# Kernel tuning notes

Hardware: AMD Instinct MI355X
Metric: run time of the kernel (lower is better)

## Reference

```python
import jax, jax.numpy as jnp
import numpy as np

# ---- pywt filter banks (dec_lo, dec_hi, rec_lo, rec_hi), all pywt-ordered ----
_SQ2 = 0.7071067811865476

def _orth(dec_lo):
    dec_lo = np.asarray(dec_lo, dtype=np.float64)
    rec_lo = dec_lo[::-1].copy()
    k = np.arange(len(dec_lo))
    dec_hi = ((-1.0) ** (k + 1)) * rec_lo
    rec_hi = dec_hi[::-1].copy()
    return dec_lo, dec_hi, rec_lo, rec_hi

_DB4 = [-0.010597401784997278, 0.032883011666982945, 0.030841381835986965,
        -0.18703481171888114, -0.02798376941698385, 0.6308807679295904,
        0.7148465705525415, 0.23037781330885523]
_SYM6 = [-0.007800708325034148, 0.0017677118642428036, 0.04472490177066578,
         -0.021060292512300564, -0.07263752278646252, 0.3379294217276218,
         0.787641141030194, 0.4910559419267466, -0.048311742585633,
         -0.11799011114819057, 0.0034907120842174702, 0.015404109327027373]
_BIOR13 = (
    np.array([-0.08838834764831845, 0.08838834764831845, _SQ2, _SQ2, 0.08838834764831845, -0.08838834764831845]),
    np.array([0.0, 0.0, -_SQ2, _SQ2, 0.0, 0.0]),
    np.array([0.0, 0.0, _SQ2, _SQ2, 0.0, 0.0]),
    np.array([-0.08838834764831845, -0.08838834764831845, _SQ2, -_SQ2, 0.08838834764831845, 0.08838834764831845]),
)

WAVELETS = ['haar', 'db4', 'sym6', 'bior1.3']
FILTERS = {
    'haar': _orth([_SQ2, _SQ2]),
    'db4': _orth(_DB4),
    'sym6': _orth(_SYM6),
    'bior1.3': _BIOR13,
}
FILTERS = {k: tuple(jnp.asarray(f, dtype=jnp.float32) for f in v) for k, v in FILTERS.items()}


def _dwt(x, dec_lo, dec_hi):
    # x: [B, C, T] (T even). ptwt: reflect-pad (2L-3)//2 each side, stride-2 corr with flipped dec filters.
    B, C, T = x.shape
    L = dec_lo.shape[0]
    p = (2 * L - 3) // 2
    xp = jnp.pad(x, ((0, 0), (0, 0), (p, p)), mode='reflect') if p > 0 else x
    filt = jnp.stack([dec_lo[::-1], dec_hi[::-1]])[:, None, :].astype(x.dtype)  # [2,1,L]
    out = jax.lax.conv_general_dilated(
        xp.reshape(B * C, 1, -1), filt, window_strides=(2,), padding='VALID',
        dimension_numbers=('NCH', 'OIH', 'NCH'))
    out = out.reshape(B, C, 2, -1)
    return out[:, :, 0], out[:, :, 1]  # approx, detail: [B, C, (T+L-2)//2]


def _idwt(lo, hi, rec_lo, rec_hi):
    # conv_transpose stride 2 with rec filters, then crop (2L-3)//2 per side (ptwt waverec).
    B, C, Tc = lo.shape
    L = rec_lo.shape[0]
    p = (2 * L - 3) // 2
    c = jnp.stack([lo, hi], axis=2).reshape(B * C, 2, Tc)
    filt = jnp.stack([rec_lo[::-1], rec_hi[::-1]])[None].astype(lo.dtype)  # [1,2,L]
    y = jax.lax.conv_general_dilated(
        c, filt, window_strides=(1,), padding=[(L - 1, L - 1)],
        lhs_dilation=(2,), dimension_numbers=('NCH', 'OIH', 'NCH'))
    y = y.reshape(B, C, -1)
    if p > 0:
        y = y[:, :, p:-p]
    return y


def _spectral(z, lam, gamma, cos_theta):
    return gamma * jnp.sign(z) * jax.nn.relu(jnp.abs(z) - lam) * cos_theta


def setup_inputs() -> dict:
    key = jax.random.key(0)
    ks = jax.random.split(key, 8)
    B, S, E = 8, 4096, 1024
    x = jax.random.normal(ks[0], (B, S, E), dtype=jnp.float32)
    lambda_approx = jnp.full((1, E, 1), 0.05, jnp.float32) + 0.01 * jax.random.uniform(ks[1], (1, E, 1), jnp.float32)
    lambda_detail = jnp.full((1, E, 1), 0.05, jnp.float32) + 0.01 * jax.random.uniform(ks[2], (1, E, 1), jnp.float32)
    log_gamma = 0.1 * jax.random.normal(ks[3], (1, E, 1), jnp.float32)
    theta = 0.1 * jax.random.normal(ks[4], (1, E, 1), jnp.float32)
    basis_logits = 0.5 * jax.random.normal(ks[5], (4,), jnp.float32)
    ln_weight = jnp.ones((E,), jnp.float32)
    ln_bias = jnp.zeros((E,), jnp.float32)
    return {'x': x, 'lambda_approx': lambda_approx, 'lambda_detail': lambda_detail,
            'log_gamma': log_gamma, 'theta': theta, 'basis_logits': basis_logits,
            'ln_weight': ln_weight, 'ln_bias': ln_bias}


def reference(x, lambda_approx, lambda_detail, log_gamma, theta, basis_logits, ln_weight, ln_bias):
    residual = x                       # [B, S, E]
    S = x.shape[1]
    xt = jnp.transpose(x, (0, 2, 1))   # [B, E, S]
    gamma = jax.nn.softplus(log_gamma) + 1e-6
    ct = jnp.cos(theta)
    weights = jax.nn.softmax(basis_logits)  # all 4 wavelets valid for even S
    out = jnp.zeros_like(xt)
    for i, name in enumerate(WAVELETS):
        dl, dh, rl, rh = FILTERS[name]
        lo, hi = _dwt(xt, dl, dh)
        lo = _spectral(lo, lambda_approx, gamma, ct)
        hi = _spectral(hi, lambda_detail, gamma, ct)
        rec = _idwt(lo, hi, rl, rh)[:, :, :S]
        out = out + weights[i] * rec
    y = jnp.transpose(out, (0, 2, 1)) + residual
    mu = jnp.mean(y, axis=-1, keepdims=True)
    var = jnp.var(y, axis=-1, keepdims=True)
    return (y - mu) / jnp.sqrt(var + 1e-5) * ln_weight + ln_bias
```

## Files before the change

### kernel.cpp

```cpp
#include <hip/hip_runtime.h>
#include <cstdint>

#define T_SEQ 4096
#define E_DIM 1024
#define N_B   8
#define SC    64
#define TILE_P 84
typedef float v2f __attribute__((ext_vector_type(2)));

constexpr int LW[4] = {2, 8, 12, 6};

constexpr float DLf[4][12] = {
  {0.7071067811865476f, 0.7071067811865476f, 0,0,0,0,0,0,0,0,0,0},
  {-0.010597401784997278f, 0.032883011666982945f, 0.030841381835986965f, -0.18703481171888114f,
   -0.02798376941698385f, 0.6308807679295904f, 0.7148465705525415f, 0.23037781330885523f, 0,0,0,0},
  {-0.007800708325034148f, 0.0017677118642428036f, 0.04472490177066578f, -0.021060292512300564f,
   -0.07263752278646252f, 0.3379294217276218f, 0.787641141030194f, 0.4910559419267466f,
   -0.048311742585633f, -0.11799011114819057f, 0.0034907120842174702f, 0.015404109327027373f},
  {-0.08838834764831845f, 0.08838834764831845f, 0.7071067811865476f, 0.7071067811865476f,
    0.08838834764831845f, -0.08838834764831845f, 0,0,0,0,0,0},
};
constexpr float DHf[4][12] = {
  {-0.7071067811865476f, 0.7071067811865476f, 0,0,0,0,0,0,0,0,0,0},
  {-0.23037781330885523f, 0.7148465705525415f, -0.6308807679295904f, -0.02798376941698385f,
    0.18703481171888114f, 0.030841381835986965f, -0.032883011666982945f, -0.010597401784997278f, 0,0,0,0},
  {-0.015404109327027373f, 0.0034907120842174702f, 0.11799011114819057f, -0.048311742585633f,
   -0.4910559419267466f, 0.787641141030194f, -0.3379294217276218f, -0.07263752278646252f,
    0.021060292512300564f, 0.04472490177066578f, -0.0017677118642428036f, -0.007800708325034148f},
  {0,0,-0.7071067811865476f, 0.7071067811865476f, 0,0, 0,0,0,0,0,0},
};
constexpr float RLf[4][12] = {
  {0.7071067811865476f, 0.7071067811865476f, 0,0,0,0,0,0,0,0,0,0},
  {0.23037781330885523f, 0.7148465705525415f, 0.6308807679295904f, -0.02798376941698385f,
   -0.18703481171888114f, 0.030841381835986965f, 0.032883011666982945f, -0.010597401784997278f, 0,0,0,0},
  {0.015404109327027373f, 0.0034907120842174702f, -0.11799011114819057f, -0.048311742585633f,
   0.4910559419267466f, 0.787641141030194f, 0.3379294217276218f, -0.07263752278646252f,
   -0.021060292512300564f, 0.04472490177066578f, 0.0017677118642428036f, -0.007800708325034148f},
  {0,0,0.7071067811865476f, 0.7071067811865476f, 0,0, 0,0,0,0,0,0},
};
constexpr float RHf[4][12] = {
  {0.7071067811865476f, -0.7071067811865476f, 0,0,0,0,0,0,0,0,0,0},
  {-0.010597401784997278f, -0.032883011666982945f, 0.030841381835986965f, 0.18703481171888114f,
   -0.02798376941698385f, -0.6308807679295904f, 0.7148465705525415f, -0.23037781330885523f, 0,0,0,0},
  {-0.007800708325034148f, -0.0017677118642428036f, 0.04472490177066578f, 0.021060292512300564f,
   -0.07263752278646252f, -0.3379294217276218f, 0.787641141030194f, -0.4910559419267466f,
   -0.048311742585633f, 0.11799011114819057f, 0.0034907120842174702f, -0.015404109327027373f},
  {-0.08838834764831845f, -0.08838834764831845f, 0.7071067811865476f, -0.7071067811865476f,
    0.08838834764831845f, 0.08838834764831845f, 0,0,0,0,0,0},
};

__device__ __forceinline__ v2f sv(float c) { return v2f{c, c}; }

template <int W>
__device__ __forceinline__ void wavelet_accum(const v2f (&xw)[36], v2f (&acc)[16],
                                              v2f la, v2f ld, v2f gw) {
  constexpr int L  = LW[W];
  constexpr int KT = L / 2 + 7;
#pragma unroll
  for (int kk = 0; kk < KT; ++kk) {
    v2f lo = {0.f, 0.f}, hi = {0.f, 0.f};
#pragma unroll
    for (int m = 0; m < L; ++m) {
      const v2f xv = xw[2 * kk + 11 - m];
      if (DLf[W][m] != 0.0f) lo += sv(DLf[W][m]) * xv;
      if (DHf[W][m] != 0.0f) hi += sv(DHf[W][m]) * xv;
    }
    v2f cl, ch;
    cl.x = __builtin_amdgcn_fmed3f(lo.x, -la.x, la.x);
    cl.y = __builtin_amdgcn_fmed3f(lo.y, -la.y, la.y);
    ch.x = __builtin_amdgcn_fmed3f(hi.x, -ld.x, ld.x);
    ch.y = __builtin_amdgcn_fmed3f(hi.y, -ld.y, ld.y);
    const v2f loS = (lo - cl) * gw;
    const v2f hiS = (hi - ch) * gw;
#pragma unroll
    for (int m = 0; m < L; ++m) {
      const int j = 2 * kk + m + 2 - L;
      if (j >= 0 && j < 16) {
        if (RLf[W][m] != 0.0f) acc[j] += loS * sv(RLf[W][m]);
        if (RHf[W][m] != 0.0f) acc[j] += hiS * sv(RHf[W][m]);
      }
    }
  }
}

__global__ __launch_bounds__(256, 3) void wlm_k1(
    const float* __restrict__ x,
    const float* __restrict__ la_, const float* __restrict__ ld_,
    const float* __restrict__ lg_, const float* __restrict__ th_,
    const float* __restrict__ bl_, float* __restrict__ y) {
  __shared__ float xs[TILE_P][2][64];

  const int tid  = threadIdx.x;
  const int lane = tid & 63;
  const int wave = tid >> 6;
  const int s0 = blockIdx.x * SC;
  const int e0 = blockIdx.y * 128;
  const int b  = blockIdx.z;

  {
    const int c4  = (tid & 31) * 4;
    const int sel = c4 >> 6;
    const int cc  = c4 & 63;
    const int prow = tid >> 5;
#pragma unroll
    for (int it = 0; it < 11; ++it) {
      const int pos = prow + it * 8;
      if (pos < TILE_P) {
        int g = s0 - 10 + pos;
        g = (g < 0) ? -g : g;
        g = (g >= T_SEQ) ? (2 * T_SEQ - 2 - g) : g;
        const float4 v = *reinterpret_cast<const float4*>(
            &x[((size_t)b * T_SEQ + g) * E_DIM + e0 + c4]);
        *reinterpret_cast<float4*>(&xs[pos][sel][cc]) = v;
      }
    }
  }

  const int e = e0 + lane, e2 = e + 64;
  const v2f la = {la_[e], la_[e2]};
  const v2f ld = {ld_[e], ld_[e2]};
  const v2f lg = {lg_[e], lg_[e2]};
  const v2f th = {th_[e], th_[e2]};
  v2f g2;
  g2.x = (fmaxf(lg.x, 0.f) + log1pf(expf(-fabsf(lg.x))) + 1e-6f) * cosf(th.x);
  g2.y = (fmaxf(lg.y, 0.f) + log1pf(expf(-fabsf(lg.y))) + 1e-6f) * cosf(th.y);

  const float b0 = bl_[0], b1 = bl_[1], b2 = bl_[2], b3 = bl_[3];
  const float mx = fmaxf(fmaxf(b0, b1), fmaxf(b2, b3));
  const float w0 = expf(b0 - mx), w1 = expf(b1 - mx),
              w2 = expf(b2 - mx), w3 = expf(b3 - mx);
  const float wr = 1.f / (w0 + w1 + w2 + w3);
  const v2f gw0 = g2 * sv(w0 * wr), gw1 = g2 * sv(w1 * wr),
            gw2 = g2 * sv(w2 * wr), gw3 = g2 * sv(w3 * wr);

  __syncthreads();

  const int base = wave * 16;
  v2f xw[36];
#pragma unroll
  for (int i = 0; i < 36; ++i) {
    xw[i] = v2f{xs[base + i][0][lane], xs[base + i][1][lane]};
  }

  v2f acc[16];
#pragma unroll
  for (int j = 0; j < 16; ++j) acc[j] = v2f{0.f, 0.f};

  wavelet_accum<0>(xw, acc, la, ld, gw0);
  wavelet_accum<1>(xw, acc, la, ld, gw1);
  wavelet_accum<2>(xw, acc, la, ld, gw2);
  wavelet_accum<3>(xw, acc, la, ld, gw3);

  const int sA = s0 + wave * 16;
#pragma unroll
  for (int j = 0; j < 16; ++j) {
    const v2f o = xw[j + 10] + acc[j];
    const size_t off = ((size_t)b * T_SEQ + sA + j) * E_DIM + e;
    y[off]      = o.x;
    y[off + 64] = o.y;
  }
}

__global__ __launch_bounds__(256) void wlm_k2(float* __restrict__ y,
                                              const float* __restrict__ w,
                                              const float* __restrict__ bias) {
  const int token = blockIdx.x;
  const int tid = threadIdx.x;
  float* row = y + (size_t)token * E_DIM;

  float4 v = *reinterpret_cast<const float4*>(&row[tid * 4]);
  float s  = v.x + v.y + v.z + v.w;
  float sq = v.x * v.x + v.y * v.y + v.z * v.z + v.w * v.w;
#pragma unroll
  for (int off = 32; off; off >>= 1) {
    s  += __shfl_down(s, off);
    sq += __shfl_down(sq, off);
  }
  __shared__ float ps[4], pq[4], stat[2];
  const int wave = tid >> 6, lane = tid & 63;
  if (lane == 0) { ps[wave] = s; pq[wave] = sq; }
  __syncthreads();
  if (tid == 0) {
    const float S1 = ps[0] + ps[1] + ps[2] + ps[3];
    const float S2 = pq[0] + pq[1] + pq[2] + pq[3];
    const float mu = S1 * (1.f / E_DIM);
    const float var = S2 * (1.f / E_DIM) - mu * mu;
    stat[0] = mu;
    stat[1] = rsqrtf(var + 1e-5f);
  }
  __syncthreads();
  const float mu = stat[0], rstd = stat[1];
  const float4 wv = *reinterpret_cast<const float4*>(&w[tid * 4]);
  const float4 bv = *reinterpret_cast<const float4*>(&bias[tid * 4]);
  float4 o;
  o.x = (v.x - mu) * rstd * wv.x + bv.x;
  o.y = (v.y - mu) * rstd * wv.y + bv.y;
  o.z = (v.z - mu) * rstd * wv.z + bv.z;
  o.w = (v.w - mu) * rstd * wv.w + bv.w;
  *reinterpret_cast<float4*>(&row[tid * 4]) = o;
}

extern "C" void kernel_launch(void* const* d_in, const int* in_sizes, int n_in,
                              void* d_out, int out_size, void* d_ws, size_t ws_size,
                              hipStream_t stream) {
  const float* x   = (const float*)d_in[0];
  const float* la  = (const float*)d_in[1];
  const float* ldt = (const float*)d_in[2];
  const float* lg  = (const float*)d_in[3];
  const float* th  = (const float*)d_in[4];
  const float* bl  = (const float*)d_in[5];
  const float* lnw = (const float*)d_in[6];
  const float* lnb = (const float*)d_in[7];
  float* out = (float*)d_out;

  dim3 g1(T_SEQ / SC, E_DIM / 128, N_B);
  wlm_k1<<<g1, 256, 0, stream>>>(x, la, ldt, lg, th, bl, out);
  wlm_k2<<<dim3(N_B * T_SEQ), 256, 0, stream>>>(out, lnw, lnb);
}
```

Measured before the change: 114.1 us.

## Load input halo directly into registers instead of staging through LDS

The shared-memory tile and its barrier are gone. Each wave now loads its own 36-row halo window straight from global memory into registers as float2 per lane, with adjacent channels assigned to a lane. Stores also become float2 and occupancy is raised to 4 blocks per CU. Each wave re-reads its 20-row overlap with neighbouring waves from global memory, relying on cache hits, in return for dropping the LDS traffic and the sync.

```diff
diff --git a/kernel.cpp b/kernel.cpp
--- a/kernel.cpp
+++ b/kernel.cpp
@@ -5,7 +5,6 @@
 #define E_DIM 1024
 #define N_B   8
 #define SC    64
-#define TILE_P 84
 typedef float v2f __attribute__((ext_vector_type(2)));
 
 constexpr int LW[4] = {2, 8, 12, 6};
@@ -83,44 +82,34 @@
   }
 }
 
-__global__ __launch_bounds__(256, 3) void wlm_k1(
+__global__ __launch_bounds__(256, 4) void wlm_k1(
     const float* __restrict__ x,
     const float* __restrict__ la_, const float* __restrict__ ld_,
     const float* __restrict__ lg_, const float* __restrict__ th_,
     const float* __restrict__ bl_, float* __restrict__ y) {
-  __shared__ float xs[TILE_P][2][64];
-
   const int tid  = threadIdx.x;
   const int lane = tid & 63;
   const int wave = tid >> 6;
   const int s0 = blockIdx.x * SC;
   const int e0 = blockIdx.y * 128;
   const int b  = blockIdx.z;
+  const int e  = e0 + 2 * lane;
+  const int sA = s0 + wave * 16;
 
-  {
-    const int c4  = (tid & 31) * 4;
-    const int sel = c4 >> 6;
-    const int cc  = c4 & 63;
-    const int prow = tid >> 5;
+  const size_t rowb = (size_t)b * T_SEQ;
+  v2f xw[36];
 #pragma unroll
-    for (int it = 0; it < 11; ++it) {
-      const int pos = prow + it * 8;
-      if (pos < TILE_P) {
-        int g = s0 - 10 + pos;
-        g = (g < 0) ? -g : g;
-        g = (g >= T_SEQ) ? (2 * T_SEQ - 2 - g) : g;
-        const float4 v = *reinterpret_cast<const float4*>(
-            &x[((size_t)b * T_SEQ + g) * E_DIM + e0 + c4]);
-        *reinterpret_cast<float4*>(&xs[pos][sel][cc]) = v;
-      }
-    }
+  for (int i = 0; i < 36; ++i) {
+    int g = sA - 10 + i;
+    g = (g < 0) ? -g : g;
+    g = (g >= T_SEQ) ? (2 * T_SEQ - 2 - g) : g;
+    xw[i] = *reinterpret_cast<const v2f*>(&x[(rowb + g) * E_DIM + e]);
   }
 
-  const int e = e0 + lane, e2 = e + 64;
-  const v2f la = {la_[e], la_[e2]};
-  const v2f ld = {ld_[e], ld_[e2]};
-  const v2f lg = {lg_[e], lg_[e2]};
-  const v2f th = {th_[e], th_[e2]};
+  const v2f la = *reinterpret_cast<const v2f*>(&la_[e]);
+  const v2f ld = *reinterpret_cast<const v2f*>(&ld_[e]);
+  const v2f lg = *reinterpret_cast<const v2f*>(&lg_[e]);
+  const v2f th = *reinterpret_cast<const v2f*>(&th_[e]);
   v2f g2;
   g2.x = (fmaxf(lg.x, 0.f) + log1pf(expf(-fabsf(lg.x))) + 1e-6f) * cosf(th.x);
   g2.y = (fmaxf(lg.y, 0.f) + log1pf(expf(-fabsf(lg.y))) + 1e-6f) * cosf(th.y);
@@ -133,15 +122,6 @@
   const v2f gw0 = g2 * sv(w0 * wr), gw1 = g2 * sv(w1 * wr),
             gw2 = g2 * sv(w2 * wr), gw3 = g2 * sv(w3 * wr);
 
-  __syncthreads();
-
-  const int base = wave * 16;
-  v2f xw[36];
-#pragma unroll
-  for (int i = 0; i < 36; ++i) {
-    xw[i] = v2f{xs[base + i][0][lane], xs[base + i][1][lane]};
-  }
-
   v2f acc[16];
 #pragma unroll
   for (int j = 0; j < 16; ++j) acc[j] = v2f{0.f, 0.f};
@@ -151,13 +131,10 @@
   wavelet_accum<2>(xw, acc, la, ld, gw2);
   wavelet_accum<3>(xw, acc, la, ld, gw3);
 
-  const int sA = s0 + wave * 16;
 #pragma unroll
   for (int j = 0; j < 16; ++j) {
     const v2f o = xw[j + 10] + acc[j];
-    const size_t off = ((size_t)b * T_SEQ + sA + j) * E_DIM + e;
-    y[off]      = o.x;
-    y[off + 64] = o.y;
+    *reinterpret_cast<v2f*>(&y[(rowb + sA + j) * E_DIM + e]) = o;
   }
 }
 
```

Result: slower. 134.8 us (+18.1%).
